# Performance work log

Hardware: AMD Instinct MI355X
Metric: run time of the kernel (lower is better)

The kernel has to match this reference:

```python
import jax, jax.numpy as jnp
import numpy as np

ALPHA = 1.702  # sigmoid-GLU scale
LIMIT = 7.0    # clamp limit
TOP_K = 2      # num_experts_per_tok


def setup_inputs() -> dict:
    key = jax.random.key(0)
    ks = jax.random.split(key, 4)
    B, S, H, E, I = 2, 1024, 1024, 8, 2048
    return {
        "hidden_states": jax.random.normal(ks[0], (B, S, H), jnp.float32),
        "router_weight": jax.random.normal(ks[1], (E, H), jnp.float32),
        "router_bias": jnp.zeros((E,), jnp.float32),
        "gate_up_proj": jax.random.normal(ks[2], (E, H, 2 * I), jnp.float32) * 0.02,
        "gate_up_bias": jnp.zeros((E, 2 * I), jnp.float32),
        "down_proj": jax.random.normal(ks[3], (E, I, H), jnp.float32) * 0.02,
        "down_bias": jnp.zeros((E, H), jnp.float32),
    }


def reference(hidden_states, router_weight, router_bias, gate_up_proj,
              gate_up_bias, down_proj, down_bias):
    B, S, H = hidden_states.shape
    E, _, two_I = gate_up_proj.shape
    I = two_I // 2

    flat = hidden_states.reshape(B * S, H)  # [T, H]

    # Router: softmax + top-k
    logits = flat @ router_weight.T + router_bias            # [T, E]
    scores = jax.nn.softmax(logits, axis=-1)
    topk_w, topk_idx = jax.lax.top_k(scores, TOP_K)          # [T, K]

    # Dense per-expert gated FFN (einsum 'abmh,ehn->abemn' computes all experts
    # on all tokens; the reshape/permute dance is a mathematical no-op).
    gu = jnp.einsum('th,ehn->ten', flat, gate_up_proj) + gate_up_bias  # [T, E, 2I]
    gate = jnp.minimum(gu[..., :I], LIMIT)
    up = jnp.clip(gu[..., I:], -LIMIT, LIMIT)
    glu = gate * jax.nn.sigmoid(gate * ALPHA)
    act = (up + 1.0) * glu                                   # [T, E, I]

    down = jnp.einsum('tei,eih->teh', act, down_proj) + down_bias  # [T, E, H]

    # Combine: gather each token's top-k expert outputs, weighted sum.
    gathered = jnp.take_along_axis(down, topk_idx[:, :, None], axis=1)  # [T, K, H]
    out = (gathered * topk_w[:, :, None]).sum(axis=1)        # [T, H]
    return out.reshape(B, S, H)
```

## Files before the change

kernel.cpp:

```cpp
#include <hip/hip_runtime.h>
#include <math.h>

#define TT 2048
#define HH 1024
#define EE 8
#define II 2048
#define N1 4096
#define ALPHA 1.702f
#define LIMIT 7.0f
#define MAXSCHED 40
#define SPLITK 2

typedef __attribute__((ext_vector_type(8))) short short8;
typedef __attribute__((ext_vector_type(4))) float floatx4;

#define GLL(g, l) __builtin_amdgcn_global_load_lds(                          \
    (const __attribute__((address_space(1))) void*)(g),                      \
    (__attribute__((address_space(3))) void*)(l), 16, 0, 0)

__device__ __forceinline__ short f2bf(float f) {
  union { float f; unsigned u; } v; v.f = f;
  unsigned r = (v.u + 0x7fffu + ((v.u >> 16) & 1u)) >> 16;
  return (short)r;
}
__device__ __forceinline__ float bf2f(unsigned short s) {
  union { unsigned u; float f; } v; v.u = ((unsigned)s) << 16;
  return v.f;
}

__global__ __launch_bounds__(256) void convert_x(const float* __restrict__ x,
                                                 unsigned short* __restrict__ xb) {
  const size_t off = ((size_t)blockIdx.x * blockDim.x + threadIdx.x) * 8;
  const float4 v0 = *(const float4*)(x + off);
  const float4 v1 = *(const float4*)(x + off + 4);
  short8 s;
  s[0]=f2bf(v0.x); s[1]=f2bf(v0.y); s[2]=f2bf(v0.z); s[3]=f2bf(v0.w);
  s[4]=f2bf(v1.x); s[5]=f2bf(v1.y); s[6]=f2bf(v1.z); s[7]=f2bf(v1.w);
  *(short8*)(xb + off) = s;
}

__global__ __launch_bounds__(256) void transpose_cvt(const float* __restrict__ src,
                                                     unsigned short* __restrict__ dst,
                                                     int K, int N) {
  const int e = blockIdx.z;
  src += (size_t)e * K * N;
  dst += (size_t)e * K * N;
  const int k0 = blockIdx.y * 64, n0 = blockIdx.x * 64;
  __shared__ unsigned short Ts[64][66];
  const int tid = threadIdx.x;
  const int c4 = (tid & 15) * 4;
  const int r = tid >> 4;
#pragma unroll
  for (int i = 0; i < 4; i++) {
    const int kk = r + i * 16;
    const float4 v = *(const float4*)(src + (size_t)(k0 + kk) * N + n0 + c4);
    Ts[kk][c4 + 0] = (unsigned short)f2bf(v.x);
    Ts[kk][c4 + 1] = (unsigned short)f2bf(v.y);
    Ts[kk][c4 + 2] = (unsigned short)f2bf(v.z);
    Ts[kk][c4 + 3] = (unsigned short)f2bf(v.w);
  }
  __syncthreads();
#pragma unroll
  for (int i = 0; i < 4; i++) {
    const int nn = r + i * 16;
    unsigned short o[4];
#pragma unroll
    for (int j = 0; j < 4; j++) o[j] = Ts[c4 + j][nn];
    *(uint2*)(dst + (size_t)(n0 + nn) * K + k0 + c4) = *(const uint2*)o;
  }
}

__global__ __launch_bounds__(256) void router_kernel(
    const float* __restrict__ x, const float* __restrict__ rw,
    const float* __restrict__ rb, int* __restrict__ topk_idx,
    float* __restrict__ topk_w) {
  const int t = blockIdx.x;
  const float* xr = x + (size_t)t * HH;
  const int lane = threadIdx.x & 63;
  const int wave = threadIdx.x >> 6;
  float xv[16];
#pragma unroll
  for (int i = 0; i < 16; i++) xv[i] = xr[lane + i * 64];
  __shared__ float logits[EE];
#pragma unroll
  for (int ee = 0; ee < 2; ee++) {
    const int e = wave * 2 + ee;
    const float* wr = rw + (size_t)e * HH;
    float s = 0.f;
#pragma unroll
    for (int i = 0; i < 16; i++) s += xv[i] * wr[lane + i * 64];
#pragma unroll
    for (int off = 32; off > 0; off >>= 1) s += __shfl_down(s, off, 64);
    if (lane == 0) logits[e] = s + rb[e];
  }
  __syncthreads();
  if (threadIdx.x == 0) {
    float sc[EE];
    float mx = -3.4e38f;
    for (int i = 0; i < EE; i++) mx = fmaxf(mx, logits[i]);
    float sum = 0.f;
    for (int i = 0; i < EE; i++) { sc[i] = expf(logits[i] - mx); sum += sc[i]; }
    const float inv = 1.f / sum;
    int i0 = 0;
    for (int i = 1; i < EE; i++) if (sc[i] > sc[i0]) i0 = i;
    int i1 = (i0 == 0) ? 1 : 0;
    for (int i = 0; i < EE; i++) if (i != i0 && sc[i] > sc[i1]) i1 = i;
    topk_idx[t * 2 + 0] = i0;
    topk_idx[t * 2 + 1] = i1;
    topk_w[t * 2 + 0] = sc[i0] * inv;
    topk_w[t * 2 + 1] = sc[i1] * inv;
  }
}

__global__ void assign_kernel(const int* __restrict__ topk_idx,
                              int* __restrict__ counts, int* __restrict__ rows) {
  const int id = blockIdx.x * blockDim.x + threadIdx.x;
  if (id >= TT * 2) return;
  const int e = topk_idx[id];
  const int slot = atomicAdd(&counts[e], 1);
  rows[e * TT + slot] = id;
}

__global__ void sched_kernel(const int* __restrict__ counts,
                             int* __restrict__ sched, int* __restrict__ nsched) {
  if (threadIdx.x == 0) {
    int n = 0;
    for (int e = 0; e < EE; e++) {
      const int mt = (counts[e] + 127) >> 7;
      for (int m = 0; m < mt; m++) sched[n++] = (e << 8) | m;
    }
    nsched[0] = n;
  }
}

__global__ __launch_bounds__(256) void gemm_gu(
    const unsigned short* __restrict__ x_bf,
    const unsigned short* __restrict__ gup_t,
    const float* __restrict__ gub,
    const int* __restrict__ counts, const int* __restrict__ rows,
    const int* __restrict__ sched, const int* __restrict__ nsched,
    unsigned short* __restrict__ gu) {
  const int sid = blockIdx.y;
  if (sid >= nsched[0]) return;
  const int sv = sched[sid];
  const int e = sv >> 8, mtile = sv & 255;
  const int count = counts[e] - mtile * 128;
  const int ntile = blockIdx.x;
  const int* rl = rows + e * TT + mtile * 128;

  __shared__ short As[128 * 32];
  __shared__ short Bs[128 * 32];

  const int tid = threadIdx.x;
  const int lane = tid & 63, wave = tid >> 6;
  const int quad = lane >> 4, r16 = lane & 15;
  const int wm = (wave & 1) << 6, wn = (wave >> 1) << 6;

  const int srow = lane >> 2;
  const int soct = (lane & 3) ^ (srow & 3);
  const int lr0 = wave * 32 + srow;
  const int lr1 = lr0 + 16;
  const int cr0 = (lr0 < count) ? lr0 : 0;
  const int cr1 = (lr1 < count) ? lr1 : 0;
  const unsigned short* aptr0 = x_bf + (size_t)(rl[cr0] >> 1) * HH + soct * 8;
  const unsigned short* aptr1 = x_bf + (size_t)(rl[cr1] >> 1) * HH + soct * 8;
  const unsigned short* bptr0 = gup_t + (size_t)e * N1 * HH +
                                (size_t)(ntile * 128 + lr0) * HH + soct * 8;
  const unsigned short* bptr1 = bptr0 + (size_t)16 * HH;

  short* lA0 = As + (wave * 32) * 32;
  short* lA1 = As + (wave * 32 + 16) * 32;
  short* lB0 = Bs + (wave * 32) * 32;
  short* lB1 = Bs + (wave * 32 + 16) * 32;

  const int fcol = (quad ^ (r16 & 3)) * 8;
  const short8* ap[4]; const short8* bp[4];
#pragma unroll
  for (int i = 0; i < 4; i++) {
    ap[i] = (const short8*)&As[(wm + i * 16 + r16) * 32 + fcol];
    bp[i] = (const short8*)&Bs[(wn + i * 16 + r16) * 32 + fcol];
  }

  floatx4 acc[4][4] = {};
  for (int k0 = 0; k0 < HH; k0 += 32) {
    __syncthreads();
    GLL(aptr0 + k0, lA0);
    GLL(aptr1 + k0, lA1);
    GLL(bptr0 + k0, lB0);
    GLL(bptr1 + k0, lB1);
    __syncthreads();
    short8 af[4], bf_[4];
#pragma unroll
    for (int i = 0; i < 4; i++) { af[i] = *ap[i]; bf_[i] = *bp[i]; }
#pragma unroll
    for (int i = 0; i < 4; i++)
#pragma unroll
      for (int j = 0; j < 4; j++)
        acc[i][j] = __builtin_amdgcn_mfma_f32_16x16x32_bf16(af[i], bf_[j], acc[i][j], 0, 0, 0);
  }

  const float* bias = gub + (size_t)e * N1 + ntile * 128;
#pragma unroll
  for (int i = 0; i < 4; i++) {
#pragma unroll
    for (int reg = 0; reg < 4; reg++) {
      const int rrow = wm + i * 16 + quad * 4 + reg;
      if (rrow < count) {
        const int ent = rl[rrow];
        unsigned short* orow = gu + (size_t)ent * N1 + ntile * 128;
#pragma unroll
        for (int j = 0; j < 4; j++) {
          const int c = wn + j * 16 + r16;
          orow[c] = (unsigned short)f2bf(acc[i][j][reg] + bias[c]);
        }
      }
    }
  }
}

__global__ __launch_bounds__(256) void act_kernel(const unsigned short* __restrict__ gu,
                                                  unsigned short* __restrict__ act) {
  const int id = blockIdx.x * blockDim.x + threadIdx.x;
  const int r = id >> 8;
  const int i8 = (id & 255) * 8;
  const short8 g8 = *(const short8*)(gu + (size_t)r * N1 + i8);
  const short8 u8 = *(const short8*)(gu + (size_t)r * N1 + II + i8);
  short8 o;
#pragma unroll
  for (int j = 0; j < 8; j++) {
    float g = bf2f((unsigned short)g8[j]);
    float u = bf2f((unsigned short)u8[j]);
    g = fminf(g, LIMIT);
    u = fminf(fmaxf(u, -LIMIT), LIMIT);
    const float glu = g / (1.f + expf(-g * ALPHA));
    o[j] = f2bf((u + 1.f) * glu);
  }
  *(short8*)(act + (size_t)r * II + i8) = o;
}

__global__ __launch_bounds__(256) void gemm_down(
    const unsigned short* __restrict__ act,
    const unsigned short* __restrict__ dp_t,
    const int* __restrict__ counts, const int* __restrict__ rows,
    const int* __restrict__ sched, const int* __restrict__ nsched,
    float* __restrict__ dout) {
  const int sid = blockIdx.y;
  if (sid >= nsched[0]) return;
  const int sv = sched[sid];
  const int e = sv >> 8, mtile = sv & 255;
  const int count = counts[e] - mtile * 128;
  const int ntile = blockIdx.x;
  const int kbase = blockIdx.z * (II / SPLITK);
  const int* rl = rows + e * TT + mtile * 128;

  __shared__ short As[128 * 32];
  __shared__ short Bs[128 * 32];

  const int tid = threadIdx.x;
  const int lane = tid & 63, wave = tid >> 6;
  const int quad = lane >> 4, r16 = lane & 15;
  const int wm = (wave & 1) << 6, wn = (wave >> 1) << 6;

  const int srow = lane >> 2;
  const int soct = (lane & 3) ^ (srow & 3);
  const int lr0 = wave * 32 + srow;
  const int lr1 = lr0 + 16;
  const int cr0 = (lr0 < count) ? lr0 : 0;
  const int cr1 = (lr1 < count) ? lr1 : 0;
  const unsigned short* aptr0 = act + (size_t)rl[cr0] * II + soct * 8;
  const unsigned short* aptr1 = act + (size_t)rl[cr1] * II + soct * 8;
  const unsigned short* bptr0 = dp_t + (size_t)e * HH * II +
                                (size_t)(ntile * 128 + lr0) * II + soct * 8;
  const unsigned short* bptr1 = bptr0 + (size_t)16 * II;

  short* lA0 = As + (wave * 32) * 32;
  short* lA1 = As + (wave * 32 + 16) * 32;
  short* lB0 = Bs + (wave * 32) * 32;
  short* lB1 = Bs + (wave * 32 + 16) * 32;

  const int fcol = (quad ^ (r16 & 3)) * 8;
  const short8* ap[4]; const short8* bp[4];
#pragma unroll
  for (int i = 0; i < 4; i++) {
    ap[i] = (const short8*)&As[(wm + i * 16 + r16) * 32 + fcol];
    bp[i] = (const short8*)&Bs[(wn + i * 16 + r16) * 32 + fcol];
  }

  floatx4 acc[4][4] = {};
  for (int k0 = kbase; k0 < kbase + II / SPLITK; k0 += 32) {
    __syncthreads();
    GLL(aptr0 + k0, lA0);
    GLL(aptr1 + k0, lA1);
    GLL(bptr0 + k0, lB0);
    GLL(bptr1 + k0, lB1);
    __syncthreads();
    short8 af[4], bf_[4];
#pragma unroll
    for (int i = 0; i < 4; i++) { af[i] = *ap[i]; bf_[i] = *bp[i]; }
#pragma unroll
    for (int i = 0; i < 4; i++)
#pragma unroll
      for (int j = 0; j < 4; j++)
        acc[i][j] = __builtin_amdgcn_mfma_f32_16x16x32_bf16(af[i], bf_[j], acc[i][j], 0, 0, 0);
  }

#pragma unroll
  for (int i = 0; i < 4; i++) {
#pragma unroll
    for (int reg = 0; reg < 4; reg++) {
      const int rrow = wm + i * 16 + quad * 4 + reg;
      if (rrow < count) {
        const int ent = rl[rrow];
        float* orow = dout + (size_t)ent * HH + ntile * 128;
#pragma unroll
        for (int j = 0; j < 4; j++) {
          const int c = wn + j * 16 + r16;
          atomicAdd(&orow[c], acc[i][j][reg]);
        }
      }
    }
  }
}

__global__ __launch_bounds__(256) void combine_kernel(
    const float* __restrict__ dout, const float* __restrict__ tw,
    const int* __restrict__ tidx, const float* __restrict__ db,
    float* __restrict__ out) {
  const int id = blockIdx.x * blockDim.x + threadIdx.x;
  const int t = id >> 8;
  const int h = (id & 255) * 4;
  const float w0 = tw[t * 2], w1 = tw[t * 2 + 1];
  const int e0 = tidx[t * 2], e1 = tidx[t * 2 + 1];
  const float4 a = *(const float4*)(dout + (size_t)(2 * t) * HH + h);
  const float4 b = *(const float4*)(dout + (size_t)(2 * t + 1) * HH + h);
  const float4 b0 = *(const float4*)(db + (size_t)e0 * HH + h);
  const float4 b1 = *(const float4*)(db + (size_t)e1 * HH + h);
  float4 o;
  o.x = w0 * (a.x + b0.x) + w1 * (b.x + b1.x);
  o.y = w0 * (a.y + b0.y) + w1 * (b.y + b1.y);
  o.z = w0 * (a.z + b0.z) + w1 * (b.z + b1.z);
  o.w = w0 * (a.w + b0.w) + w1 * (b.w + b1.w);
  *(float4*)(out + (size_t)t * HH + h) = o;
}

extern "C" void kernel_launch(void* const* d_in, const int* in_sizes, int n_in,
                              void* d_out, int out_size, void* d_ws, size_t ws_size,
                              hipStream_t stream) {
  const float* x   = (const float*)d_in[0];
  const float* rw  = (const float*)d_in[1];
  const float* rb  = (const float*)d_in[2];
  const float* gup = (const float*)d_in[3];
  const float* gub = (const float*)d_in[4];
  const float* dp  = (const float*)d_in[5];
  const float* db  = (const float*)d_in[6];
  float* out = (float*)d_out;

  char* ws = (char*)d_ws;
  int*   topk_idx = (int*)(ws + 0);
  float* topk_w   = (float*)(ws + 16384);
  int*   counts   = (int*)(ws + 32768);
  int*   nsched   = (int*)(ws + 33024);
  int*   sched    = (int*)(ws + 33280);
  int*   rows     = (int*)(ws + 36864);
  unsigned short* x_bf  = (unsigned short*)(ws + (1u << 20));
  unsigned short* gup_t = (unsigned short*)(ws + 8388608);
  unsigned short* act   = (unsigned short*)(ws + 8388608);
  unsigned short* dp_t  = (unsigned short*)(ws + 75497472);
  unsigned short* gu    = (unsigned short*)(ws + 109051904);
  float*          dout  = (float*)(ws + 109051904);

  convert_x<<<TT * HH / (256 * 8), 256, 0, stream>>>(x, x_bf);
  transpose_cvt<<<dim3(N1 / 64, HH / 64, EE), 256, 0, stream>>>(gup, gup_t, HH, N1);
  transpose_cvt<<<dim3(HH / 64, II / 64, EE), 256, 0, stream>>>(dp, dp_t, II, HH);
  router_kernel<<<TT, 256, 0, stream>>>(x, rw, rb, topk_idx, topk_w);
  hipMemsetAsync(counts, 0, 64, stream);
  assign_kernel<<<(TT * 2 + 255) / 256, 256, 0, stream>>>(topk_idx, counts, rows);
  sched_kernel<<<1, 64, 0, stream>>>(counts, sched, nsched);
  gemm_gu<<<dim3(N1 / 128, MAXSCHED), 256, 0, stream>>>(
      x_bf, gup_t, gub, counts, rows, sched, nsched, gu);
  act_kernel<<<TT * 2 * II / (256 * 8), 256, 0, stream>>>(gu, act);
  hipMemsetAsync(dout, 0, (size_t)TT * 2 * HH * 4, stream);
  gemm_down<<<dim3(HH / 128, MAXSCHED, SPLITK), 256, 0, stream>>>(
      act, dp_t, counts, rows, sched, nsched, dout);
  combine_kernel<<<(TT * HH / 4) / 256, 256, 0, stream>>>(dout, topk_w, topk_idx, db, out);
}
```

Before: 455.7 us.

## Read fp32 expert weights directly in GEMMs, drop transpose-convert passes

```diff
diff --git a/kernel.cpp b/kernel.cpp
--- a/kernel.cpp
+++ b/kernel.cpp
@@ -9,7 +9,6 @@
 #define ALPHA 1.702f
 #define LIMIT 7.0f
 #define MAXSCHED 40
-#define SPLITK 2
 
 typedef __attribute__((ext_vector_type(8))) short short8;
 typedef __attribute__((ext_vector_type(4))) float floatx4;
@@ -37,37 +36,6 @@
   s[0]=f2bf(v0.x); s[1]=f2bf(v0.y); s[2]=f2bf(v0.z); s[3]=f2bf(v0.w);
   s[4]=f2bf(v1.x); s[5]=f2bf(v1.y); s[6]=f2bf(v1.z); s[7]=f2bf(v1.w);
   *(short8*)(xb + off) = s;
-}
-
-__global__ __launch_bounds__(256) void transpose_cvt(const float* __restrict__ src,
-                                                     unsigned short* __restrict__ dst,
-                                                     int K, int N) {
-  const int e = blockIdx.z;
-  src += (size_t)e * K * N;
-  dst += (size_t)e * K * N;
-  const int k0 = blockIdx.y * 64, n0 = blockIdx.x * 64;
-  __shared__ unsigned short Ts[64][66];
-  const int tid = threadIdx.x;
-  const int c4 = (tid & 15) * 4;
-  const int r = tid >> 4;
-#pragma unroll
-  for (int i = 0; i < 4; i++) {
-    const int kk = r + i * 16;
-    const float4 v = *(const float4*)(src + (size_t)(k0 + kk) * N + n0 + c4);
-    Ts[kk][c4 + 0] = (unsigned short)f2bf(v.x);
-    Ts[kk][c4 + 1] = (unsigned short)f2bf(v.y);
-    Ts[kk][c4 + 2] = (unsigned short)f2bf(v.z);
-    Ts[kk][c4 + 3] = (unsigned short)f2bf(v.w);
-  }
-  __syncthreads();
-#pragma unroll
-  for (int i = 0; i < 4; i++) {
-    const int nn = r + i * 16;
-    unsigned short o[4];
-#pragma unroll
-    for (int j = 0; j < 4; j++) o[j] = Ts[c4 + j][nn];
-    *(uint2*)(dst + (size_t)(n0 + nn) * K + k0 + c4) = *(const uint2*)o;
-  }
 }
 
 __global__ __launch_bounds__(256) void router_kernel(
@@ -133,9 +101,9 @@
   }
 }
 
-__global__ __launch_bounds__(256) void gemm_gu(
+__global__ __launch_bounds__(256, 3) void gemm_gu(
     const unsigned short* __restrict__ x_bf,
-    const unsigned short* __restrict__ gup_t,
+    const float* __restrict__ gup,
     const float* __restrict__ gub,
     const int* __restrict__ counts, const int* __restrict__ rows,
     const int* __restrict__ sched, const int* __restrict__ nsched,
@@ -148,55 +116,62 @@
   const int ntile = blockIdx.x;
   const int* rl = rows + e * TT + mtile * 128;
 
-  __shared__ short As[128 * 32];
-  __shared__ short Bs[128 * 32];
+  __shared__ short As[128 * 128];
 
   const int tid = threadIdx.x;
   const int lane = tid & 63, wave = tid >> 6;
   const int quad = lane >> 4, r16 = lane & 15;
   const int wm = (wave & 1) << 6, wn = (wave >> 1) << 6;
 
-  const int srow = lane >> 2;
-  const int soct = (lane & 3) ^ (srow & 3);
-  const int lr0 = wave * 32 + srow;
-  const int lr1 = lr0 + 16;
-  const int cr0 = (lr0 < count) ? lr0 : 0;
-  const int cr1 = (lr1 < count) ? lr1 : 0;
-  const unsigned short* aptr0 = x_bf + (size_t)(rl[cr0] >> 1) * HH + soct * 8;
-  const unsigned short* aptr1 = x_bf + (size_t)(rl[cr1] >> 1) * HH + soct * 8;
-  const unsigned short* bptr0 = gup_t + (size_t)e * N1 * HH +
-                                (size_t)(ntile * 128 + lr0) * HH + soct * 8;
-  const unsigned short* bptr1 = bptr0 + (size_t)16 * HH;
-
-  short* lA0 = As + (wave * 32) * 32;
-  short* lA1 = As + (wave * 32 + 16) * 32;
-  short* lB0 = Bs + (wave * 32) * 32;
-  short* lB1 = Bs + (wave * 32 + 16) * 32;
-
-  const int fcol = (quad ^ (r16 & 3)) * 8;
-  const short8* ap[4]; const short8* bp[4];
-#pragma unroll
-  for (int i = 0; i < 4; i++) {
-    ap[i] = (const short8*)&As[(wm + i * 16 + r16) * 32 + fcol];
-    bp[i] = (const short8*)&Bs[(wn + i * 16 + r16) * 32 + fcol];
-  }
+  const unsigned short* asrc[8];
+#pragma unroll
+  for (int p = 0; p < 8; p++) {
+    const int m = wave * 32 + p * 4 + (lane >> 4);
+    const int cm = (m < count) ? m : 0;
+    const int g = (lane & 15) ^ (m & 15);
+    asrc[p] = x_bf + (size_t)(rl[cm] >> 1) * HH + g * 8;
+  }
+
+  const int nbase = ntile * 128 + wn + r16;
+  int voff[8];
+#pragma unroll
+  for (int j = 0; j < 8; j++) voff[j] = (quad * 8 + j) * N1 + nbase;
+  const float* bbase = gup + (size_t)e * HH * N1;
 
   floatx4 acc[4][4] = {};
-  for (int k0 = 0; k0 < HH; k0 += 32) {
+
+  for (int c = 0; c < 8; c++) {
     __syncthreads();
-    GLL(aptr0 + k0, lA0);
-    GLL(aptr1 + k0, lA1);
-    GLL(bptr0 + k0, lB0);
-    GLL(bptr1 + k0, lB1);
+#pragma unroll
+    for (int p = 0; p < 8; p++)
+      GLL(asrc[p] + c * 128, &As[(wave * 32 + p * 4) * 128]);
     __syncthreads();
-    short8 af[4], bf_[4];
-#pragma unroll
-    for (int i = 0; i < 4; i++) { af[i] = *ap[i]; bf_[i] = *bp[i]; }
-#pragma unroll
-    for (int i = 0; i < 4; i++)
-#pragma unroll
-      for (int j = 0; j < 4; j++)
-        acc[i][j] = __builtin_amdgcn_mfma_f32_16x16x32_bf16(af[i], bf_[j], acc[i][j], 0, 0, 0);
+#pragma unroll 2
+    for (int kt = 0; kt < 4; kt++) {
+      short8 af[4];
+#pragma unroll
+      for (int i = 0; i < 4; i++) {
+        const int m = wm + i * 16 + r16;
+        const int sl = (kt * 4 + quad) ^ r16;
+        af[i] = *(const short8*)&As[m * 128 + sl * 8];
+      }
+#pragma unroll
+      for (int f = 0; f < 4; f++) {
+        float bv[8];
+#pragma unroll
+        for (int j = 0; j < 8; j++) bv[j] = bbase[voff[j] + f * 16];
+        union { unsigned u[4]; short8 s8; } bp;
+#pragma unroll
+        for (int j = 0; j < 4; j++)
+          bp.u[j] = __builtin_amdgcn_perm(__float_as_uint(bv[2 * j + 1]),
+                                          __float_as_uint(bv[2 * j]), 0x07060302u);
+#pragma unroll
+        for (int i = 0; i < 4; i++)
+          acc[i][f] = __builtin_amdgcn_mfma_f32_16x16x32_bf16(af[i], bp.s8, acc[i][f], 0, 0, 0);
+      }
+#pragma unroll
+      for (int j = 0; j < 8; j++) voff[j] += 32 * N1;
+    }
   }
 
   const float* bias = gub + (size_t)e * N1 + ntile * 128;
@@ -209,9 +184,9 @@
         const int ent = rl[rrow];
         unsigned short* orow = gu + (size_t)ent * N1 + ntile * 128;
 #pragma unroll
-        for (int j = 0; j < 4; j++) {
-          const int c = wn + j * 16 + r16;
-          orow[c] = (unsigned short)f2bf(acc[i][j][reg] + bias[c]);
+        for (int f = 0; f < 4; f++) {
+          const int cc = wn + f * 16 + r16;
+          orow[cc] = (unsigned short)f2bf(acc[i][f][reg] + bias[cc]);
         }
       }
     }
@@ -238,9 +213,9 @@
   *(short8*)(act + (size_t)r * II + i8) = o;
 }
 
-__global__ __launch_bounds__(256) void gemm_down(
+__global__ __launch_bounds__(256, 3) void gemm_down(
     const unsigned short* __restrict__ act,
-    const unsigned short* __restrict__ dp_t,
+    const float* __restrict__ dp,
     const int* __restrict__ counts, const int* __restrict__ rows,
     const int* __restrict__ sched, const int* __restrict__ nsched,
     float* __restrict__ dout) {
@@ -250,58 +225,65 @@
   const int e = sv >> 8, mtile = sv & 255;
   const int count = counts[e] - mtile * 128;
   const int ntile = blockIdx.x;
-  const int kbase = blockIdx.z * (II / SPLITK);
+  const int kbase = blockIdx.z * (II / 4);
   const int* rl = rows + e * TT + mtile * 128;
 
-  __shared__ short As[128 * 32];
-  __shared__ short Bs[128 * 32];
+  __shared__ short As[128 * 128];
 
   const int tid = threadIdx.x;
   const int lane = tid & 63, wave = tid >> 6;
   const int quad = lane >> 4, r16 = lane & 15;
   const int wm = (wave & 1) << 6, wn = (wave >> 1) << 6;
 
-  const int srow = lane >> 2;
-  const int soct = (lane & 3) ^ (srow & 3);
-  const int lr0 = wave * 32 + srow;
-  const int lr1 = lr0 + 16;
-  const int cr0 = (lr0 < count) ? lr0 : 0;
-  const int cr1 = (lr1 < count) ? lr1 : 0;
-  const unsigned short* aptr0 = act + (size_t)rl[cr0] * II + soct * 8;
-  const unsigned short* aptr1 = act + (size_t)rl[cr1] * II + soct * 8;
-  const unsigned short* bptr0 = dp_t + (size_t)e * HH * II +
-                                (size_t)(ntile * 128 + lr0) * II + soct * 8;
-  const unsigned short* bptr1 = bptr0 + (size_t)16 * II;
-
-  short* lA0 = As + (wave * 32) * 32;
-  short* lA1 = As + (wave * 32 + 16) * 32;
-  short* lB0 = Bs + (wave * 32) * 32;
-  short* lB1 = Bs + (wave * 32 + 16) * 32;
-
-  const int fcol = (quad ^ (r16 & 3)) * 8;
-  const short8* ap[4]; const short8* bp[4];
-#pragma unroll
-  for (int i = 0; i < 4; i++) {
-    ap[i] = (const short8*)&As[(wm + i * 16 + r16) * 32 + fcol];
-    bp[i] = (const short8*)&Bs[(wn + i * 16 + r16) * 32 + fcol];
-  }
+  const unsigned short* asrc[8];
+#pragma unroll
+  for (int p = 0; p < 8; p++) {
+    const int m = wave * 32 + p * 4 + (lane >> 4);
+    const int cm = (m < count) ? m : 0;
+    const int g = (lane & 15) ^ (m & 15);
+    asrc[p] = act + (size_t)rl[cm] * II + kbase + g * 8;
+  }
+
+  const int nbase = ntile * 128 + wn + r16;
+  int voff[8];
+#pragma unroll
+  for (int j = 0; j < 8; j++) voff[j] = (kbase + quad * 8 + j) * HH + nbase;
+  const float* bbase = dp + (size_t)e * II * HH;
 
   floatx4 acc[4][4] = {};
-  for (int k0 = kbase; k0 < kbase + II / SPLITK; k0 += 32) {
+
+  for (int c = 0; c < 4; c++) {
     __syncthreads();
-    GLL(aptr0 + k0, lA0);
-    GLL(aptr1 + k0, lA1);
-    GLL(bptr0 + k0, lB0);
-    GLL(bptr1 + k0, lB1);
+#pragma unroll
+    for (int p = 0; p < 8; p++)
+      GLL(asrc[p] + c * 128, &As[(wave * 32 + p * 4) * 128]);
     __syncthreads();
-    short8 af[4], bf_[4];
-#pragma unroll
-    for (int i = 0; i < 4; i++) { af[i] = *ap[i]; bf_[i] = *bp[i]; }
-#pragma unroll
-    for (int i = 0; i < 4; i++)
-#pragma unroll
-      for (int j = 0; j < 4; j++)
-        acc[i][j] = __builtin_amdgcn_mfma_f32_16x16x32_bf16(af[i], bf_[j], acc[i][j], 0, 0, 0);
+#pragma unroll 2
+    for (int kt = 0; kt < 4; kt++) {
+      short8 af[4];
+#pragma unroll
+      for (int i = 0; i < 4; i++) {
+        const int m = wm + i * 16 + r16;
+        const int sl = (kt * 4 + quad) ^ r16;
+        af[i] = *(const short8*)&As[m * 128 + sl * 8];
+      }
+#pragma unroll
+      for (int f = 0; f < 4; f++) {
+        float bv[8];
+#pragma unroll
+        for (int j = 0; j < 8; j++) bv[j] = bbase[voff[j] + f * 16];
+        union { unsigned u[4]; short8 s8; } bp;
+#pragma unroll
+        for (int j = 0; j < 4; j++)
+          bp.u[j] = __builtin_amdgcn_perm(__float_as_uint(bv[2 * j + 1]),
+                                          __float_as_uint(bv[2 * j]), 0x07060302u);
+#pragma unroll
+        for (int i = 0; i < 4; i++)
+          acc[i][f] = __builtin_amdgcn_mfma_f32_16x16x32_bf16(af[i], bp.s8, acc[i][f], 0, 0, 0);
+      }
+#pragma unroll
+      for (int j = 0; j < 8; j++) voff[j] += 32 * HH;
+    }
   }
 
 #pragma unroll
@@ -313,9 +295,9 @@
         const int ent = rl[rrow];
         float* orow = dout + (size_t)ent * HH + ntile * 128;
 #pragma unroll
-        for (int j = 0; j < 4; j++) {
-          const int c = wn + j * 16 + r16;
-          atomicAdd(&orow[c], acc[i][j][reg]);
+        for (int f = 0; f < 4; f++) {
+          const int cc = wn + f * 16 + r16;
+          atomicAdd(&orow[cc], acc[i][f][reg]);
         }
       }
     }
@@ -362,25 +344,21 @@
   int*   nsched   = (int*)(ws + 33024);
   int*   sched    = (int*)(ws + 33280);
   int*   rows     = (int*)(ws + 36864);
-  unsigned short* x_bf  = (unsigned short*)(ws + (1u << 20));
-  unsigned short* gup_t = (unsigned short*)(ws + 8388608);
-  unsigned short* act   = (unsigned short*)(ws + 8388608);
-  unsigned short* dp_t  = (unsigned short*)(ws + 75497472);
-  unsigned short* gu    = (unsigned short*)(ws + 109051904);
-  float*          dout  = (float*)(ws + 109051904);
+  unsigned short* x_bf = (unsigned short*)(ws + (1u << 20));
+  unsigned short* gu   = (unsigned short*)(ws + 8388608);
+  unsigned short* act  = (unsigned short*)(ws + 50331648);
+  float*          dout = (float*)(ws + 75497472);
 
   convert_x<<<TT * HH / (256 * 8), 256, 0, stream>>>(x, x_bf);
-  transpose_cvt<<<dim3(N1 / 64, HH / 64, EE), 256, 0, stream>>>(gup, gup_t, HH, N1);
-  transpose_cvt<<<dim3(HH / 64, II / 64, EE), 256, 0, stream>>>(dp, dp_t, II, HH);
   router_kernel<<<TT, 256, 0, stream>>>(x, rw, rb, topk_idx, topk_w);
   hipMemsetAsync(counts, 0, 64, stream);
   assign_kernel<<<(TT * 2 + 255) / 256, 256, 0, stream>>>(topk_idx, counts, rows);
   sched_kernel<<<1, 64, 0, stream>>>(counts, sched, nsched);
   gemm_gu<<<dim3(N1 / 128, MAXSCHED), 256, 0, stream>>>(
-      x_bf, gup_t, gub, counts, rows, sched, nsched, gu);
+      x_bf, gup, gub, counts, rows, sched, nsched, gu);
   act_kernel<<<TT * 2 * II / (256 * 8), 256, 0, stream>>>(gu, act);
   hipMemsetAsync(dout, 0, (size_t)TT * 2 * HH * 4, stream);
-  gemm_down<<<dim3(HH / 128, MAXSCHED, SPLITK), 256, 0, stream>>>(
-      act, dp_t, counts, rows, sched, nsched, dout);
+  gemm_down<<<dim3(HH / 128, MAXSCHED, 4), 256, 0, stream>>>(
+      act, dp, counts, rows, sched, nsched, dout);
   combine_kernel<<<(TT * HH / 4) / 256, 256, 0, stream>>>(dout, topk_w, topk_idx, db, out);
 }
```

After: 457.2 us. No clear change (+0.3%).
